# Performance work log

Hardware: AMD Instinct MI355X
Metric: run time of the kernel (lower is better)

## Reference

```python
import jax, jax.numpy as jnp
import numpy as np
import math

INPUT_DIM = 1024
HIDDEN_DIM = 1024
NUM_HEADS = 16
NUM_KEYS = 4096
BATCH = 1024
BETA = 8.0


def setup_inputs() -> dict:
    key = jax.random.key(0)
    kx, kk, kv = jax.random.split(key, 3)
    bound_k = 1.0 / math.sqrt(INPUT_DIM)
    bound_v = 1.0 / math.sqrt(HIDDEN_DIM)
    x = jax.random.normal(kx, (BATCH, INPUT_DIM), dtype=jnp.float32)
    keys = jax.random.uniform(kk, (NUM_KEYS * NUM_HEADS, INPUT_DIM), dtype=jnp.float32,
                              minval=-bound_k, maxval=bound_k)
    values = jax.random.uniform(kv, (NUM_KEYS * NUM_HEADS, HIDDEN_DIM), dtype=jnp.float32,
                                minval=-bound_v, maxval=bound_v)
    return {"x": x, "keys": keys, "values": values}


def reference(x, keys, values):
    scale = math.sqrt(INPUT_DIM)
    b = x.shape[0]
    # [B, num_keys*num_heads]
    weights = (x @ keys.T) / scale
    # view as [B, num_keys, num_heads]; softmax over num_keys per head
    weights = weights.reshape(b, NUM_KEYS, NUM_HEADS)
    probs = jax.nn.softmax(BETA * weights, axis=1)
    probs = probs.reshape(b, NUM_KEYS * NUM_HEADS)
    # value retrieval
    out = probs @ values  # [B, hidden_dim]
    return out
```

## Files before the change

### kernel.cpp

```cpp
#include <hip/hip_runtime.h>
#include <hip/hip_bf16.h>
#include <stdint.h>

#define BATCH  1024
#define DIM    1024
#define NKH    65536
#define HID    1024

#define SC1 0.36067376022224085f

typedef __bf16 bf16x8 __attribute__((ext_vector_type(8)));
typedef float  f32x4  __attribute__((ext_vector_type(4)));

__device__ __forceinline__ unsigned short f2bf(float f) {
  union { float f; unsigned int u; } v; v.f = f;
  unsigned int r = v.u + 0x7fffu + ((v.u >> 16) & 1u);
  return (unsigned short)(r >> 16);
}
__device__ __forceinline__ float bf2f(unsigned short s) {
  union { unsigned int u; float f; } v; v.u = ((unsigned int)s) << 16;
  return v.f;
}
__device__ __forceinline__ unsigned int pk2(float lo, float hi) {
  union { __hip_bfloat162 h; unsigned int u; } v;
  v.h = __float22bfloat162_rn(make_float2(lo, hi));
  return v.u;
}

__global__ __launch_bounds__(256) void k_transpose_cast(
    const float* __restrict__ V, unsigned short* __restrict__ vT) {
  __shared__ float tile[64][65];
  const int t = threadIdx.x;
  const int nk0 = blockIdx.x * 64;
  const int j0  = blockIdx.y * 64;
  #pragma unroll
  for (int i = 0; i < 4; ++i) {
    int idx = t + i * 256;
    int row = idx >> 4, c4 = (idx & 15) << 2;
    float4 v = *(const float4*)(V + (size_t)(nk0 + row) * HID + (j0 + c4));
    tile[row][c4 + 0] = v.x; tile[row][c4 + 1] = v.y;
    tile[row][c4 + 2] = v.z; tile[row][c4 + 3] = v.w;
  }
  __syncthreads();
  const int q = t & 7, jj = t >> 3;
  #pragma unroll
  for (int i = 0; i < 2; ++i) {
    int j = jj + i * 32;
    uint4 o;
    o.x = pk2(tile[q*8+0][j], tile[q*8+1][j]);
    o.y = pk2(tile[q*8+2][j], tile[q*8+3][j]);
    o.z = pk2(tile[q*8+4][j], tile[q*8+5][j]);
    o.w = pk2(tile[q*8+6][j], tile[q*8+7][j]);
    *(uint4*)(vT + (size_t)(j0 + j) * NKH + (nk0 + q*8)) = o;
  }
}

__global__ __launch_bounds__(256) void k_gemm1_exp(
    const float* __restrict__ X, const float* __restrict__ Kp,
    unsigned short* __restrict__ E) {
  __shared__ __align__(16) unsigned short As[128 * 32];
  __shared__ __align__(16) unsigned short Bs[128 * 32];
  const int t = threadIdx.x;
  const int bm = blockIdx.x & 7, bn = blockIdx.x >> 3;
  const int m0 = bm << 7, n0 = bn << 7;
  const int rowS = t >> 1, half = t & 1;
  const float* ga = X  + (size_t)(m0 + rowS) * DIM + half * 16;
  const float* gb = Kp + (size_t)(n0 + rowS) * DIM + half * 16;
  unsigned short* wA = As + rowS * 32 + half * 16;
  unsigned short* wB = Bs + rowS * 32 + half * 16;
  const int lane = t & 63, wave = t >> 6;
  const int wm = (wave >> 1) << 6, wn = (wave & 1) << 6;
  const int r16 = lane & 15, quad = lane >> 4;
  f32x4 acc[4][4] = {};
  for (int k0 = 0; k0 < DIM; k0 += 32) {
    float4 a0 = *(const float4*)(ga + k0);
    float4 a1 = *(const float4*)(ga + k0 + 4);
    float4 a2 = *(const float4*)(ga + k0 + 8);
    float4 a3 = *(const float4*)(ga + k0 + 12);
    float4 b0 = *(const float4*)(gb + k0);
    float4 b1 = *(const float4*)(gb + k0 + 4);
    float4 b2 = *(const float4*)(gb + k0 + 8);
    float4 b3 = *(const float4*)(gb + k0 + 12);
    __syncthreads();
    uint4 w;
    w.x = pk2(a0.x, a0.y); w.y = pk2(a0.z, a0.w);
    w.z = pk2(a1.x, a1.y); w.w = pk2(a1.z, a1.w);
    *(uint4*)(wA) = w;
    w.x = pk2(a2.x, a2.y); w.y = pk2(a2.z, a2.w);
    w.z = pk2(a3.x, a3.y); w.w = pk2(a3.z, a3.w);
    *(uint4*)(wA + 8) = w;
    w.x = pk2(b0.x, b0.y); w.y = pk2(b0.z, b0.w);
    w.z = pk2(b1.x, b1.y); w.w = pk2(b1.z, b1.w);
    *(uint4*)(wB) = w;
    w.x = pk2(b2.x, b2.y); w.y = pk2(b2.z, b2.w);
    w.z = pk2(b3.x, b3.y); w.w = pk2(b3.z, b3.w);
    *(uint4*)(wB + 8) = w;
    __syncthreads();
    bf16x8 af[4], bfr[4];
    #pragma unroll
    for (int mi = 0; mi < 4; ++mi)
      af[mi] = *(const bf16x8*)(As + (wm + mi*16 + r16) * 32 + quad * 8);
    #pragma unroll
    for (int ni = 0; ni < 4; ++ni)
      bfr[ni] = *(const bf16x8*)(Bs + (wn + ni*16 + r16) * 32 + quad * 8);
    #pragma unroll
    for (int mi = 0; mi < 4; ++mi)
      #pragma unroll
      for (int ni = 0; ni < 4; ++ni)
        acc[mi][ni] = __builtin_amdgcn_mfma_f32_16x16x32_bf16(af[mi], bfr[ni], acc[mi][ni], 0, 0, 0);
  }
  #pragma unroll
  for (int mi = 0; mi < 4; ++mi) {
    #pragma unroll
    for (int ni = 0; ni < 4; ++ni) {
      #pragma unroll
      for (int v = 0; v < 4; ++v) {
        int row = m0 + wm + mi*16 + quad*4 + v;
        int col = n0 + wn + ni*16 + r16;
        E[(size_t)row * NKH + col] = f2bf(exp2f(acc[mi][ni][v] * SC1));
      }
    }
  }
}

__global__ __launch_bounds__(256) void k_row_denom(
    const unsigned short* __restrict__ E, float* __restrict__ r) {
  __shared__ float acc16[16];
  const int t = threadIdx.x, b = blockIdx.x;
  if (t < 16) acc16[t] = 0.0f;
  __syncthreads();
  float s0=0,s1=0,s2=0,s3=0,s4=0,s5=0,s6=0,s7=0;
  const unsigned short* row = E + (size_t)b * NKH;
  for (int c = t; c < NKH / 8; c += 256) {
    uint4 u = *(const uint4*)(row + c * 8);
    s0 += bf2f((unsigned short)(u.x & 0xffff)); s1 += bf2f((unsigned short)(u.x >> 16));
    s2 += bf2f((unsigned short)(u.y & 0xffff)); s3 += bf2f((unsigned short)(u.y >> 16));
    s4 += bf2f((unsigned short)(u.z & 0xffff)); s5 += bf2f((unsigned short)(u.z >> 16));
    s6 += bf2f((unsigned short)(u.w & 0xffff)); s7 += bf2f((unsigned short)(u.w >> 16));
  }
  const int h0 = (t & 1) * 8;
  atomicAdd(&acc16[h0 + 0], s0); atomicAdd(&acc16[h0 + 1], s1);
  atomicAdd(&acc16[h0 + 2], s2); atomicAdd(&acc16[h0 + 3], s3);
  atomicAdd(&acc16[h0 + 4], s4); atomicAdd(&acc16[h0 + 5], s5);
  atomicAdd(&acc16[h0 + 6], s6); atomicAdd(&acc16[h0 + 7], s7);
  __syncthreads();
  if (t < 16) r[b * 16 + t] = 1.0f / acc16[t];
}

__global__ __launch_bounds__(256) void k_scale(
    unsigned short* __restrict__ E, const float* __restrict__ r) {
  const int t = threadIdx.x, b = blockIdx.x;
  const int h0 = (t & 1) * 8;
  float rr[8];
  #pragma unroll
  for (int i = 0; i < 8; ++i) rr[i] = r[b * 16 + h0 + i];
  unsigned short* row = E + (size_t)b * NKH;
  for (int c = t; c < NKH / 8; c += 256) {
    uint4 u = *(uint4*)(row + c * 8);
    uint4 o;
    o.x = pk2(bf2f((unsigned short)(u.x & 0xffff)) * rr[0],
              bf2f((unsigned short)(u.x >> 16))    * rr[1]);
    o.y = pk2(bf2f((unsigned short)(u.y & 0xffff)) * rr[2],
              bf2f((unsigned short)(u.y >> 16))    * rr[3]);
    o.z = pk2(bf2f((unsigned short)(u.z & 0xffff)) * rr[4],
              bf2f((unsigned short)(u.z >> 16))    * rr[5]);
    o.w = pk2(bf2f((unsigned short)(u.w & 0xffff)) * rr[6],
              bf2f((unsigned short)(u.w >> 16))    * rr[7]);
    *(uint4*)(row + c * 8) = o;
  }
}

__device__ __forceinline__ void gl2lds16(const void* g, void* l) {
  __builtin_amdgcn_global_load_lds(
      (const __attribute__((address_space(1))) void*)g,
      (__attribute__((address_space(3))) void*)l, 16, 0, 0);
}

__global__ __launch_bounds__(256) void k_gemm2(
    const unsigned short* __restrict__ P, const unsigned short* __restrict__ Vt,
    float* __restrict__ out) {
  __shared__ __align__(16) unsigned short As[128 * 32];
  __shared__ __align__(16) unsigned short Bs[128 * 32];
  const int t = threadIdx.x;
  const int bm = blockIdx.x & 7, bn = (blockIdx.x >> 3) & 7, sp = blockIdx.x >> 6;
  const int m0 = bm << 7, n0 = bn << 7;
  const size_t kb = (size_t)sp * (NKH / 16);
  const int lane = t & 63, wave = t >> 6;
  const int wm = (wave >> 1) << 6, wn = (wave & 1) << 6;
  const int r16 = lane & 15, quad = lane >> 4;
  const int srow = lane >> 2, kseg = (lane & 3) * 8;
  const int c0 = wave * 2, c1 = wave * 2 + 1;
  const unsigned short* gA0 = P  + (size_t)(m0 + c0*16 + srow) * NKH + kb + kseg;
  const unsigned short* gA1 = P  + (size_t)(m0 + c1*16 + srow) * NKH + kb + kseg;
  const unsigned short* gB0 = Vt + (size_t)(n0 + c0*16 + srow) * NKH + kb + kseg;
  const unsigned short* gB1 = Vt + (size_t)(n0 + c1*16 + srow) * NKH + kb + kseg;
  f32x4 acc[4][4] = {};
  for (int ks = 0; ks < NKH / 16; ks += 32) {
    __syncthreads();
    gl2lds16(gA0 + ks, As + c0 * 512);
    gl2lds16(gA1 + ks, As + c1 * 512);
    gl2lds16(gB0 + ks, Bs + c0 * 512);
    gl2lds16(gB1 + ks, Bs + c1 * 512);
    __syncthreads();
    bf16x8 af[4], bfr[4];
    #pragma unroll
    for (int mi = 0; mi < 4; ++mi)
      af[mi] = *(const bf16x8*)(As + (wm + mi*16 + r16) * 32 + quad * 8);
    #pragma unroll
    for (int ni = 0; ni < 4; ++ni)
      bfr[ni] = *(const bf16x8*)(Bs + (wn + ni*16 + r16) * 32 + quad * 8);
    #pragma unroll
    for (int mi = 0; mi < 4; ++mi)
      #pragma unroll
      for (int ni = 0; ni < 4; ++ni)
        acc[mi][ni] = __builtin_amdgcn_mfma_f32_16x16x32_bf16(af[mi], bfr[ni], acc[mi][ni], 0, 0, 0);
  }
  #pragma unroll
  for (int mi = 0; mi < 4; ++mi) {
    #pragma unroll
    for (int ni = 0; ni < 4; ++ni) {
      #pragma unroll
      for (int v = 0; v < 4; ++v) {
        int row = m0 + wm + mi*16 + quad*4 + v;
        int col = n0 + wn + ni*16 + r16;
        unsafeAtomicAdd(&out[(size_t)row * HID + col], acc[mi][ni][v]);
      }
    }
  }
}

extern "C" void kernel_launch(void* const* d_in, const int* in_sizes, int n_in,
                              void* d_out, int out_size, void* d_ws, size_t ws_size,
                              hipStream_t stream) {
  (void)in_sizes; (void)n_in; (void)out_size; (void)ws_size;
  const float* x      = (const float*)d_in[0];
  const float* keys   = (const float*)d_in[1];
  const float* values = (const float*)d_in[2];
  float* out = (float*)d_out;

  unsigned short* E  = (unsigned short*)d_ws;
  unsigned short* vT = E + (size_t)BATCH * NKH;
  float* r = (float*)(vT + (size_t)HID * NKH);

  hipMemsetAsync(d_out, 0, (size_t)BATCH * HID * sizeof(float), stream);
  k_transpose_cast<<<dim3(NKH / 64, HID / 64), 256, 0, stream>>>(values, vT);
  k_gemm1_exp<<<(BATCH / 128) * (NKH / 128), 256, 0, stream>>>(x, keys, E);
  k_row_denom<<<BATCH, 256, 0, stream>>>(E, r);
  k_scale<<<BATCH, 256, 0, stream>>>(E, r);
  k_gemm2<<<(BATCH / 128) * (HID / 128) * 16, 256, 0, stream>>>(E, vT, out);
}
```

Baseline: 1.208 ms.

## Pre-cast keys and x to bf16 and load GEMM1 tiles via global_load_lds

Adds a bf16 cast pass for keys and x so GEMM1 reads half the bytes per tile and loads them straight into LDS with global_load_lds, instead of loading fp32, converting in registers and storing to LDS. The workspace buffer used for transposed values is reused for the casted keys, and the value transpose now runs after the softmax kernels. This adds extra cast kernels, with full reads and writes of keys, in exchange for a leaner GEMM1 inner loop. The LDS layout changes to the 16-row chunk format already used by GEMM2.

```diff
diff --git a/kernel.cpp b/kernel.cpp
--- a/kernel.cpp
+++ b/kernel.cpp
@@ -25,6 +25,23 @@
   union { __hip_bfloat162 h; unsigned int u; } v;
   v.h = __float22bfloat162_rn(make_float2(lo, hi));
   return v.u;
+}
+__device__ __forceinline__ void gl2lds16(const void* g, void* l) {
+  __builtin_amdgcn_global_load_lds(
+      (const __attribute__((address_space(1))) void*)g,
+      (__attribute__((address_space(3))) void*)l, 16, 0, 0);
+}
+
+__global__ __launch_bounds__(256) void k_cast(
+    const float* __restrict__ s, unsigned short* __restrict__ d, int n8) {
+  int i = blockIdx.x * 256 + threadIdx.x;
+  if (i >= n8) return;
+  float4 a = ((const float4*)s)[(size_t)i * 2];
+  float4 b = ((const float4*)s)[(size_t)i * 2 + 1];
+  uint4 o;
+  o.x = pk2(a.x, a.y); o.y = pk2(a.z, a.w);
+  o.z = pk2(b.x, b.y); o.w = pk2(b.z, b.w);
+  ((uint4*)d)[i] = o;
 }
 
 __global__ __launch_bounds__(256) void k_transpose_cast(
@@ -56,45 +73,29 @@
 }
 
 __global__ __launch_bounds__(256) void k_gemm1_exp(
-    const float* __restrict__ X, const float* __restrict__ Kp,
+    const unsigned short* __restrict__ Xb, const unsigned short* __restrict__ Kb,
     unsigned short* __restrict__ E) {
   __shared__ __align__(16) unsigned short As[128 * 32];
   __shared__ __align__(16) unsigned short Bs[128 * 32];
   const int t = threadIdx.x;
   const int bm = blockIdx.x & 7, bn = blockIdx.x >> 3;
   const int m0 = bm << 7, n0 = bn << 7;
-  const int rowS = t >> 1, half = t & 1;
-  const float* ga = X  + (size_t)(m0 + rowS) * DIM + half * 16;
-  const float* gb = Kp + (size_t)(n0 + rowS) * DIM + half * 16;
-  unsigned short* wA = As + rowS * 32 + half * 16;
-  unsigned short* wB = Bs + rowS * 32 + half * 16;
   const int lane = t & 63, wave = t >> 6;
   const int wm = (wave >> 1) << 6, wn = (wave & 1) << 6;
   const int r16 = lane & 15, quad = lane >> 4;
+  const int srow = lane >> 2, kseg = (lane & 3) * 8;
+  const int c0 = wave * 2, c1 = wave * 2 + 1;
+  const unsigned short* gA0 = Xb + (size_t)(m0 + c0*16 + srow) * DIM + kseg;
+  const unsigned short* gA1 = Xb + (size_t)(m0 + c1*16 + srow) * DIM + kseg;
+  const unsigned short* gB0 = Kb + (size_t)(n0 + c0*16 + srow) * DIM + kseg;
+  const unsigned short* gB1 = Kb + (size_t)(n0 + c1*16 + srow) * DIM + kseg;
   f32x4 acc[4][4] = {};
-  for (int k0 = 0; k0 < DIM; k0 += 32) {
-    float4 a0 = *(const float4*)(ga + k0);
-    float4 a1 = *(const float4*)(ga + k0 + 4);
-    float4 a2 = *(const float4*)(ga + k0 + 8);
-    float4 a3 = *(const float4*)(ga + k0 + 12);
-    float4 b0 = *(const float4*)(gb + k0);
-    float4 b1 = *(const float4*)(gb + k0 + 4);
-    float4 b2 = *(const float4*)(gb + k0 + 8);
-    float4 b3 = *(const float4*)(gb + k0 + 12);
-    __syncthreads();
-    uint4 w;
-    w.x = pk2(a0.x, a0.y); w.y = pk2(a0.z, a0.w);
-    w.z = pk2(a1.x, a1.y); w.w = pk2(a1.z, a1.w);
-    *(uint4*)(wA) = w;
-    w.x = pk2(a2.x, a2.y); w.y = pk2(a2.z, a2.w);
-    w.z = pk2(a3.x, a3.y); w.w = pk2(a3.z, a3.w);
-    *(uint4*)(wA + 8) = w;
-    w.x = pk2(b0.x, b0.y); w.y = pk2(b0.z, b0.w);
-    w.z = pk2(b1.x, b1.y); w.w = pk2(b1.z, b1.w);
-    *(uint4*)(wB) = w;
-    w.x = pk2(b2.x, b2.y); w.y = pk2(b2.z, b2.w);
-    w.z = pk2(b3.x, b3.y); w.w = pk2(b3.z, b3.w);
-    *(uint4*)(wB + 8) = w;
+  for (int ks = 0; ks < DIM; ks += 32) {
+    __syncthreads();
+    gl2lds16(gA0 + ks, As + c0 * 512);
+    gl2lds16(gA1 + ks, As + c1 * 512);
+    gl2lds16(gB0 + ks, Bs + c0 * 512);
+    gl2lds16(gB1 + ks, Bs + c1 * 512);
     __syncthreads();
     bf16x8 af[4], bfr[4];
     #pragma unroll
@@ -168,12 +169,6 @@
               bf2f((unsigned short)(u.w >> 16))    * rr[7]);
     *(uint4*)(row + c * 8) = o;
   }
-}
-
-__device__ __forceinline__ void gl2lds16(const void* g, void* l) {
-  __builtin_amdgcn_global_load_lds(
-      (const __attribute__((address_space(1))) void*)g,
-      (__attribute__((address_space(3))) void*)l, 16, 0, 0);
 }
 
 __global__ __launch_bounds__(256) void k_gemm2(
@@ -239,13 +234,16 @@
   float* out = (float*)d_out;
 
   unsigned short* E  = (unsigned short*)d_ws;
-  unsigned short* vT = E + (size_t)BATCH * NKH;
-  float* r = (float*)(vT + (size_t)HID * NKH);
+  unsigned short* B2 = E + (size_t)BATCH * NKH;
+  unsigned short* Xb = B2 + (size_t)NKH * DIM;
+  float* r = (float*)(Xb + (size_t)BATCH * DIM);
 
   hipMemsetAsync(d_out, 0, (size_t)BATCH * HID * sizeof(float), stream);
-  k_transpose_cast<<<dim3(NKH / 64, HID / 64), 256, 0, stream>>>(values, vT);
-  k_gemm1_exp<<<(BATCH / 128) * (NKH / 128), 256, 0, stream>>>(x, keys, E);
+  k_cast<<<(NKH * (DIM / 8) + 255) / 256, 256, 0, stream>>>(keys, B2, NKH * (DIM / 8));
+  k_cast<<<(BATCH * (DIM / 8) + 255) / 256, 256, 0, stream>>>(x, Xb, BATCH * (DIM / 8));
+  k_gemm1_exp<<<(BATCH / 128) * (NKH / 128), 256, 0, stream>>>(Xb, B2, E);
   k_row_denom<<<BATCH, 256, 0, stream>>>(E, r);
   k_scale<<<BATCH, 256, 0, stream>>>(E, r);
-  k_gemm2<<<(BATCH / 128) * (HID / 128) * 16, 256, 0, stream>>>(E, vT, out);
-}
+  k_transpose_cast<<<dim3(NKH / 64, HID / 64), 256, 0, stream>>>(values, B2);
+  k_gemm2<<<(BATCH / 128) * (HID / 128) * 16, 256, 0, stream>>>(E, B2, out);
+}
```

Result: faster. 1.138 ms (-5.8%).
